# Kernel tuning notes

Hardware: AMD Instinct MI355X
Metric: run time of the kernel (lower is better)

The kernel has to match this reference:

```python
import jax, jax.numpy as jnp
from jax import lax
import numpy as np

jax.config.update("jax_enable_x64", True)  # coder state needs 32-bit unsigned range in int64

FULL = 1 << 32
HALF = FULL >> 1
QUARTER = HALF >> 1
THREE_Q = 3 * QUARTER
RANGE_MASK = FULL - 1
CTX_BITS = 8
N_STATES = 1 << CTX_BITS
STATE_MASK = N_STATES - 1
PRECISION = 12
TOTAL = 1 << PRECISION
MAXBITS = 1 << 21


def _context_freqs(bits):
    # Adaptive per-context P(bit=0) frequencies, sequential over the bit stream.
    def step(carry, bit):
        c0, c1, state = carry
        a = c0[state]
        b = c1[state]
        p0 = a.astype(jnp.float64) / (a + b).astype(jnp.float64)
        f = jnp.clip(jnp.rint(p0 * (TOTAL - 2)) + 1.0, 1.0, TOTAL - 1.0).astype(jnp.int64)
        c0 = c0.at[state].add(1 - bit)
        c1 = c1.at[state].add(bit)
        state = ((state << 1) | bit) & STATE_MASK
        return (c0, c1, state), f

    init = (jnp.ones(N_STATES, jnp.int64), jnp.ones(N_STATES, jnp.int64), jnp.int64(0))
    _, freqs = lax.scan(step, init, bits)
    return freqs


def _arith_encode(bits, freqs):
    # Binary arithmetic coder with carry-pending renormalization.
    def renorm_cond(c):
        low, high, pending, buf, ptr = c
        return (high < HALF) | (low >= HALF) | ((low >= QUARTER) & (high < THREE_Q))

    def renorm_body(c):
        low, high, pending, buf, ptr = c
        is_a = high < HALF                      # emit 0
        is_b = (~is_a) & (low >= HALF)          # emit 1
        do_emit = is_a | is_b
        outbit = is_b.astype(jnp.uint8)
        n_write = jnp.where(do_emit, 1 + pending, jnp.int64(0))

        def wbody(i, b):
            return b.at[ptr + i].set(jnp.where(i == 0, outbit, 1 - outbit))

        buf = lax.fori_loop(0, n_write, wbody, buf)
        ptr = ptr + n_write
        pending = jnp.where(do_emit, jnp.int64(0), pending + 1)
        shift = jnp.where(is_a, jnp.int64(0), jnp.where(is_b, jnp.int64(HALF), jnp.int64(QUARTER)))
        low = ((low - shift) << 1) & RANGE_MASK
        high = (((high - shift) << 1) & RANGE_MASK) | 1
        return (low, high, pending, buf, ptr)

    def step(carry, inp):
        low, high, pending, buf, ptr = carry
        bit, p0 = inp
        rng = high - low + 1
        split = low + (rng * p0) // TOTAL
        high = jnp.where(bit == 0, split - 1, high)
        low = jnp.where(bit == 0, low, split)
        carry = lax.while_loop(renorm_cond, renorm_body, (low, high, pending, buf, ptr))
        return carry, None

    init = (jnp.int64(0), jnp.int64(FULL - 1), jnp.int64(0),
            jnp.zeros(MAXBITS, jnp.uint8), jnp.int64(0))
    (low, high, pending, buf, ptr), _ = lax.scan(step, init, (bits, freqs))

    # flush: pending += 1 then emit final bit + pending complements
    pending = pending + 1
    final_bit = (low >= QUARTER).astype(jnp.uint8)
    buf = buf.at[ptr].set(final_bit)
    buf = lax.fori_loop(0, pending, lambda i, b: b.at[ptr + 1 + i].set(1 - final_bit), buf)
    ptr = ptr + 1 + pending

    # packbits MSB-first (bitorder='big'); trailing buffer bits are zero, matching numpy's zero-padding
    w = jnp.array([128, 64, 32, 16, 8, 4, 2, 1], jnp.int64)
    packed = (buf.reshape(-1, 8).astype(jnp.int64) * w).sum(-1).astype(jnp.uint8)
    return packed, ptr


def setup_inputs() -> dict:
    key = jax.random.key(0)
    raw = jax.random.randint(key, (1024, 1024), 0, 2)
    symbols = (2 * raw - 1).astype(jnp.float32)  # values in {-1, +1}
    return {"symbols": symbols}


def reference(symbols):
    bits = ((symbols.reshape(-1) + 1.0) * 0.5).astype(jnp.uint8).astype(jnp.int64)
    freqs = _context_freqs(bits)
    packed, nbits = _arith_encode(bits, freqs)
    return packed, nbits
```

## Files before the change

kernel.cpp:

```cpp
#include <hip/hip_runtime.h>
#include <hip/hip_bf16.h>


#define N_TOT (1 << 20)
#define BLK_ELEMS 4096
#define N_BLKS (N_TOT / BLK_ELEMS)
#define NLIMB 65552

__global__ void k_keys(const float* __restrict__ sym, unsigned short* __restrict__ keys) {
    int t = blockIdx.x * blockDim.x + threadIdx.x;
    if (t >= N_TOT) return;
    unsigned s = 0;
#pragma unroll
    for (int i = 1; i <= 8; ++i) {
        unsigned b = (t >= i) ? (sym[t - i] > 0.0f ? 1u : 0u) : 0u;
        s |= b << (i - 1);
    }
    unsigned bit = sym[t] > 0.0f ? 1u : 0u;
    keys[t] = (unsigned short)((s << 1) | bit);
}

__global__ void k_hist(const unsigned short* __restrict__ keys, unsigned* __restrict__ histG) {
    __shared__ unsigned h[512];
    for (int i = threadIdx.x; i < 512; i += blockDim.x) h[i] = 0;
    __syncthreads();
    int base = blockIdx.x * BLK_ELEMS;
    for (int i = threadIdx.x; i < BLK_ELEMS; i += blockDim.x)
        atomicAdd(&h[keys[base + i]], 1u);
    __syncthreads();
    for (int i = threadIdx.x; i < 512; i += blockDim.x)
        histG[blockIdx.x * 512 + i] = h[i];
}

__global__ void k_scan(const unsigned* __restrict__ histG, unsigned* __restrict__ offsG) {
    int k = blockIdx.x * blockDim.x + threadIdx.x;
    if (k >= 512) return;
    unsigned run = 0;
    for (int b = 0; b < N_BLKS; ++b) {
        offsG[b * 512 + k] = run;
        run += histG[b * 512 + k];
    }
}

__global__ __launch_bounds__(64) void k_freq(const unsigned short* __restrict__ keys,
                                             const unsigned* __restrict__ offsG,
                                             unsigned short* __restrict__ fb) {
    __shared__ unsigned cnt[512];
    int lane = threadIdx.x;
    for (int i = lane; i < 512; i += 64) cnt[i] = offsG[blockIdx.x * 512 + i];
    __syncthreads();
    int base = blockIdx.x * BLK_ELEMS;
    unsigned long long ltm = (1ull << lane) - 1ull;
    for (int c = 0; c < BLK_ELEMS / 64; ++c) {
        int t = base + c * 64 + lane;
        unsigned key = keys[t];
        unsigned bit = key & 1u;
        unsigned state = key >> 1;
        unsigned long long eq = ~0ull;
#pragma unroll
        for (int b = 0; b < 8; ++b) {
            unsigned long long mb = __ballot((state >> b) & 1u);
            eq &= ((state >> b) & 1u) ? mb : ~mb;
        }
        unsigned long long bb = __ballot(bit);
        unsigned long long same = eq & (bit ? bb : ~bb);
        unsigned long long sib  = eq & (bit ? ~bb : bb);
        unsigned base_same = cnt[key];
        unsigned base_sib  = cnt[key ^ 1u];
        __syncthreads();
        unsigned c_same = base_same + (unsigned)__popcll(same & ltm);
        unsigned c_sib  = base_sib  + (unsigned)__popcll(sib & ltm);
        unsigned long long a0 = 1ull + (unsigned long long)(bit ? c_sib : c_same);
        unsigned long long a1 = 1ull + (unsigned long long)(bit ? c_same : c_sib);
        double p0 = (double)a0 / (double)(a0 + a1);
        double fd = rint(p0 * 4094.0) + 1.0;
        fd = fd < 1.0 ? 1.0 : (fd > 4095.0 ? 4095.0 : fd);
        unsigned f = (unsigned)fd;
        fb[t] = (unsigned short)(f | (bit << 15));
        int hi = 63 - __builtin_clzll(same);
        if (lane == hi) cnt[key] = base_same + (unsigned)__popcll(same);
        __syncthreads();
    }
}

__global__ void k_zerol(unsigned long long* __restrict__ limb) {
    int i = blockIdx.x * 256 + threadIdx.x;
    if (i < NLIMB) limb[i] = 0ull;
}

#define SYM(W, FI, BP) \
  "s_bfe_u32 s22, " W ", " FI "\n\t"           \
  "s_mul_i32 s20, s24, s22\n\t"                \
  "s_mul_hi_u32 s21, s24, s22\n\t"             \
  "s_add_u32 s20, s20, s22\n\t"                \
  "s_addc_u32 s21, s21, 0\n\t"                                      \
  "s_lshr_b64 s[20:21], s[20:21], 12\n\t"      \
  "s_add_u32 s26, %[lo], s20\n\t"              \
  "s_add_u32 s27, s26, -1\n\t"                 \
  "s_bitcmp1_b32 " W ", " BP "\n\t"            \
  "s_cselect_b32 %[lo], s26, %[lo]\n\t"        \
  "s_cselect_b32 %[hi], %[hi], s27\n\t"        \
  "s_xor_b32 s28, %[lo], %[hi]\n\t"            \
  "s_flbit_i32_b32 s29, s28\n\t"               \
  "s_andn2_b32 s30, %[lo], %[hi]\n\t"          \
  "s_add_u32 s31, s29, 1\n\t"                                       \
  "s_lshl_b32 s30, s30, s31\n\t"               \
  "s_and_b32 s34, s30, 0x80000000\n\t"         \
  "s_not_b32 s32, s30\n\t"                                          \
  "s_flbit_i32_b32 s33, s32\n\t"               \
  "s_add_u32 s29, s29, s33\n\t"                \
  "s_add_u32 %[pp], %[pp], s29\n\t"                                 \
  "s_lshl_b32 %[lo], %[lo], s29\n\t"                                \
  "s_lshl_b32 %[hi], %[hi], s29\n\t"                                \
  "s_lshl_b32 s35, 1, s29\n\t"                                      \
  "s_xor_b32 %[lo], %[lo], s34\n\t"                                 \
  "s_add_u32 s35, s35, -1\n\t"                 \
  "s_add_u32 %[hi], %[hi], s35\n\t"                                 \
  "s_xor_b32 %[hi], %[hi], s34\n\t"                                 \
  "s_sub_u32 s24, %[hi], %[lo]\n\t"

#define SYM2(W) SYM(W, "0x000C0000", "15") SYM(W, "0x000C0010", "31")

__global__ __launch_bounds__(64) void k_enc4(const unsigned short* __restrict__ fb,
                                             uint4* __restrict__ bnd,
                                             unsigned* __restrict__ hdr) {
    if (threadIdx.x != 0 || blockIdx.x != 0) return;
    unsigned low = 0u, high = 0xFFFFFFFFu, pp = 0u;
    const uint4* pq = (const uint4*)fb;
    uint4 A = pq[0], B = pq[1];
    const int NC = N_TOT / 16;
    for (int cc = 0; cc < NC; ++cc) {
        if ((cc & 15) == 0) bnd[cc >> 4] = make_uint4(low, high, pp, 0u);
        unsigned w0 = __builtin_amdgcn_readfirstlane(A.x);
        unsigned w1 = __builtin_amdgcn_readfirstlane(A.y);
        unsigned w2 = __builtin_amdgcn_readfirstlane(A.z);
        unsigned w3 = __builtin_amdgcn_readfirstlane(A.w);
        unsigned w4 = __builtin_amdgcn_readfirstlane(B.x);
        unsigned w5 = __builtin_amdgcn_readfirstlane(B.y);
        unsigned w6 = __builtin_amdgcn_readfirstlane(B.z);
        unsigned w7 = __builtin_amdgcn_readfirstlane(B.w);
        if (cc + 1 < NC) { A = pq[2 * cc + 2]; B = pq[2 * cc + 3]; }
        asm volatile(
            "s_sub_u32 s24, %[hi], %[lo]\n\t"
            SYM2("%[w0]") SYM2("%[w1]") SYM2("%[w2]") SYM2("%[w3]")
            SYM2("%[w4]") SYM2("%[w5]") SYM2("%[w6]") SYM2("%[w7]")
            : [lo]"+s"(low), [hi]"+s"(high), [pp]"+s"(pp)
            : [w0]"s"(w0), [w1]"s"(w1), [w2]"s"(w2), [w3]"s"(w3),
              [w4]"s"(w4), [w5]"s"(w5), [w6]"s"(w6), [w7]"s"(w7)
            : "s20","s21","s22","s23","s24","s25","s26","s27","s28","s29",
              "s30","s31","s32","s33","s34","s35","scc");
    }
    hdr[1] = pp;
}

__global__ __launch_bounds__(256) void k_chunk(const unsigned short* __restrict__ fb,
                                               const uint4* __restrict__ bnd,
                                               const unsigned* __restrict__ hdr,
                                               unsigned long long* __restrict__ limb) {
    int c = blockIdx.x * 256 + threadIdx.x;
    uint4 s = bnd[c];
    unsigned low = s.x, high = s.y, pp = s.z;
    unsigned pend = hdr[1];
    const unsigned* fw = (const unsigned*)fb;
    int base = c * 256;
    for (int i = 0; i < 256; i += 2) {
        unsigned w = fw[(base + i) >> 1];
#pragma unroll
        for (int h = 0; h < 2; ++h) {
            unsigned val = (w >> (h * 16)) & 0xFFFFu;
            unsigned f = val & 0xFFFu;
            unsigned bitv = val >> 15;
            unsigned r = high - low;
            unsigned long long prod = (unsigned long long)r * f + f;
            unsigned d = (unsigned)(prod >> 12);
            unsigned split = low + d;
            if (bitv) {
                unsigned sh = pend - pp;
                unsigned long long v = (unsigned long long)d << (sh & 31u);
                unsigned j = sh >> 5;
                atomicAdd(&limb[j], v & 0xFFFFFFFFull);
                unsigned long long vh = v >> 32;
                if (vh) atomicAdd(&limb[j + 1], vh);
            }
            high = bitv ? high : (split - 1u);
            low  = bitv ? split : low;
            unsigned D = low ^ high;
            unsigned k = (unsigned)__builtin_clz(D);
            unsigned kp1 = k + 1u;
            unsigned m = (unsigned)__builtin_clz((~(low << kp1)) | (high << kp1));
            unsigned K = k + m;
            pp += K;
            unsigned sub = m ? 0x80000000u : 0u;
            low  = (low << K) ^ sub;
            high = ((high << K) + ((1u << K) - 1u)) ^ sub;
        }
    }
}

__global__ __launch_bounds__(64) void k_carry2(const unsigned long long* __restrict__ limb,
                                               unsigned* __restrict__ res,
                                               unsigned* __restrict__ hdr) {
    if (threadIdx.x != 0 || blockIdx.x != 0) return;
    unsigned long long c = 0ull;
    const uint4* lp = (const uint4*)limb;
    unsigned first = 0;
    for (int b = 0; b < NLIMB / 16; ++b) {
        uint4 q[8];
#pragma unroll
        for (int u = 0; u < 8; ++u) q[u] = lp[b * 8 + u];
#pragma unroll
        for (int u = 0; u < 8; ++u) {
            unsigned long long l0 = (unsigned long long)q[u].x | ((unsigned long long)q[u].y << 32);
            unsigned long long l1 = (unsigned long long)q[u].z | ((unsigned long long)q[u].w << 32);
            unsigned long long t = l0 + c;
            res[b * 16 + 2 * u] = (unsigned)t; c = t >> 32;
            t = l1 + c;
            res[b * 16 + 2 * u + 1] = (unsigned)t; c = t >> 32;
            if (b == 0 && u == 0) first = res[0];
        }
    }
    unsigned fbit = (first >> 30) & 1u;
    res[0] = 1u << (30u + fbit);
    hdr[0] = hdr[1] + 2u;
}

__global__ void k_out2(const unsigned* __restrict__ res,
                       const unsigned* __restrict__ hdr, int* __restrict__ out) {
    int q = blockIdx.x * blockDim.x + threadIdx.x;
    if (q > 262144) return;
    unsigned nbits = hdr[0];
    if (q == 262144) { out[q] = (int)nbits; return; }
    if ((unsigned)(8 * q) >= nbits) { out[q] = 0; return; }
    unsigned pend = nbits - 2u;
    unsigned t = pend + 24u - 8u * (unsigned)q;
    unsigned j = t >> 5, o = t & 31u;
    unsigned long long w = (unsigned long long)res[j] | ((unsigned long long)res[j + 1] << 32);
    out[q] = (int)((w >> o) & 0xFFu);
}

extern "C" void kernel_launch(void* const* d_in, const int* in_sizes, int n_in,
                              void* d_out, int out_size, void* d_ws, size_t ws_size,
                              hipStream_t stream) {
    (void)in_sizes; (void)n_in; (void)out_size; (void)ws_size;
    const float* sym = (const float*)d_in[0];
    int* out = (int*)d_out;
    char* ws = (char*)d_ws;
    unsigned*            hdr   = (unsigned*)(ws);
    unsigned*            histG = (unsigned*)(ws + 266240);
    unsigned*            offsG = (unsigned*)(ws + 790528);
    unsigned short*      keys  = (unsigned short*)(ws + 1314816);
    unsigned short*      fb    = (unsigned short*)(ws + 3411968);
    unsigned long long*  limb  = (unsigned long long*)(ws + 266240);
    unsigned*            res   = (unsigned*)(ws + 790656);
    uint4*               bnd   = (uint4*)(ws + 1314816);

    k_keys<<<N_TOT / 256, 256, 0, stream>>>(sym, keys);
    k_hist<<<N_BLKS, 256, 0, stream>>>(keys, histG);
    k_scan<<<1, 512, 0, stream>>>(histG, offsG);
    k_freq<<<N_BLKS, 64, 0, stream>>>(keys, offsG, fb);
    k_zerol<<<(NLIMB + 255) / 256, 256, 0, stream>>>(limb);
    k_enc4<<<1, 64, 0, stream>>>(fb, bnd, hdr);
    k_chunk<<<16, 256, 0, stream>>>(fb, bnd, hdr, limb);
    k_carry2<<<1, 64, 0, stream>>>(limb, res, hdr);
    k_out2<<<1025, 256, 0, stream>>>(res, hdr, out);
}
```

Before: 61.17 ms.

## Drop bit-count tracking from serial scalar encoder; recover it with parallel chunk pass and scan

The single-thread scalar arithmetic-coder pass no longer accumulates the output bit position. It only records low/high at chunk boundaries, and it now processes 32 symbols per iteration. A new parallel pass re-encodes each chunk to count its emitted bits, and a scan turns those counts into per-chunk bit offsets and the total for the final pass. The renormalization sequence is also shortened by folding the mask into a shift of high+1, and constants are moved into SGPRs. The aim is to shorten the serial critical path, which dominates runtime, at the cost of an extra parallel pass and two extra launches.

```diff
diff --git a/kernel.cpp b/kernel.cpp
--- a/kernel.cpp
+++ b/kernel.cpp
@@ -93,44 +93,42 @@
   "s_mul_i32 s20, s24, s22\n\t"                \
   "s_mul_hi_u32 s21, s24, s22\n\t"             \
   "s_add_u32 s20, s20, s22\n\t"                \
-  "s_addc_u32 s21, s21, 0\n\t"                                      \
+  "s_addc_u32 s21, s21, 0\n\t"                                             \
   "s_lshr_b64 s[20:21], s[20:21], 12\n\t"      \
   "s_add_u32 s26, %[lo], s20\n\t"              \
   "s_add_u32 s27, s26, -1\n\t"                 \
   "s_bitcmp1_b32 " W ", " BP "\n\t"            \
-  "s_cselect_b32 %[lo], s26, %[lo]\n\t"        \
-  "s_cselect_b32 %[hi], %[hi], s27\n\t"        \
-  "s_xor_b32 s28, %[lo], %[hi]\n\t"            \
+  "s_cselect_b32 %[lo], s26, %[lo]\n\t"                                    \
+  "s_cselect_b32 %[hi], %[hi], s27\n\t"                                    \
+  "s_xor_b32 s28, %[lo], %[hi]\n\t"                                        \
   "s_flbit_i32_b32 s29, s28\n\t"               \
-  "s_andn2_b32 s30, %[lo], %[hi]\n\t"          \
-  "s_add_u32 s31, s29, 1\n\t"                                       \
+  "s_andn2_b32 s30, %[lo], %[hi]\n\t"                                      \
+  "s_add_u32 s31, s29, 1\n\t"                                              \
   "s_lshl_b32 s30, s30, s31\n\t"               \
-  "s_and_b32 s34, s30, 0x80000000\n\t"         \
-  "s_not_b32 s32, s30\n\t"                                          \
+  "s_and_b32 s34, s30, %[msk]\n\t"             \
+  "s_not_b32 s32, s30\n\t"                                                 \
   "s_flbit_i32_b32 s33, s32\n\t"               \
   "s_add_u32 s29, s29, s33\n\t"                \
-  "s_add_u32 %[pp], %[pp], s29\n\t"                                 \
-  "s_lshl_b32 %[lo], %[lo], s29\n\t"                                \
-  "s_lshl_b32 %[hi], %[hi], s29\n\t"                                \
-  "s_lshl_b32 s35, 1, s29\n\t"                                      \
-  "s_xor_b32 %[lo], %[lo], s34\n\t"                                 \
-  "s_add_u32 s35, s35, -1\n\t"                 \
-  "s_add_u32 %[hi], %[hi], s35\n\t"                                 \
-  "s_xor_b32 %[hi], %[hi], s34\n\t"                                 \
+  "s_lshl_b32 %[lo], %[lo], s29\n\t"                                       \
+  "s_add_u32 %[hi], %[hi], 1\n\t"              \
+  "s_lshl_b32 %[hi], %[hi], s29\n\t"                                       \
+  "s_xor_b32 %[lo], %[lo], s34\n\t"                                        \
+  "s_add_u32 %[hi], %[hi], -1\n\t"             \
+  "s_xor_b32 %[hi], %[hi], s34\n\t"                                        \
   "s_sub_u32 s24, %[hi], %[lo]\n\t"
 
-#define SYM2(W) SYM(W, "0x000C0000", "15") SYM(W, "0x000C0010", "31")
-
-__global__ __launch_bounds__(64) void k_enc4(const unsigned short* __restrict__ fb,
-                                             uint4* __restrict__ bnd,
-                                             unsigned* __restrict__ hdr) {
+#define SYM2(W) SYM(W, "%[c0]", "15") SYM(W, "%[c1]", "31")
+
+__global__ __launch_bounds__(64) void k_enc5(const unsigned short* __restrict__ fb,
+                                             uint2* __restrict__ bnd) {
     if (threadIdx.x != 0 || blockIdx.x != 0) return;
-    unsigned low = 0u, high = 0xFFFFFFFFu, pp = 0u;
+    unsigned low = 0u, high = 0xFFFFFFFFu;
+    unsigned c0 = 0x000C0000u, c1 = 0x000C0010u, mk = 0x80000000u;
     const uint4* pq = (const uint4*)fb;
-    uint4 A = pq[0], B = pq[1];
-    const int NC = N_TOT / 16;
+    uint4 A = pq[0], B = pq[1], C = pq[2], D = pq[3];
+    const int NC = N_TOT / 32;
     for (int cc = 0; cc < NC; ++cc) {
-        if ((cc & 15) == 0) bnd[cc >> 4] = make_uint4(low, high, pp, 0u);
+        if ((cc & 7) == 0) bnd[cc >> 3] = make_uint2(low, high);
         unsigned w0 = __builtin_amdgcn_readfirstlane(A.x);
         unsigned w1 = __builtin_amdgcn_readfirstlane(A.y);
         unsigned w2 = __builtin_amdgcn_readfirstlane(A.z);
@@ -139,27 +137,107 @@
         unsigned w5 = __builtin_amdgcn_readfirstlane(B.y);
         unsigned w6 = __builtin_amdgcn_readfirstlane(B.z);
         unsigned w7 = __builtin_amdgcn_readfirstlane(B.w);
-        if (cc + 1 < NC) { A = pq[2 * cc + 2]; B = pq[2 * cc + 3]; }
+        unsigned w8 = __builtin_amdgcn_readfirstlane(C.x);
+        unsigned w9 = __builtin_amdgcn_readfirstlane(C.y);
+        unsigned wa = __builtin_amdgcn_readfirstlane(C.z);
+        unsigned wb = __builtin_amdgcn_readfirstlane(C.w);
+        unsigned wc = __builtin_amdgcn_readfirstlane(D.x);
+        unsigned wd = __builtin_amdgcn_readfirstlane(D.y);
+        unsigned we = __builtin_amdgcn_readfirstlane(D.z);
+        unsigned wf = __builtin_amdgcn_readfirstlane(D.w);
+        if (cc + 1 < NC) {
+            A = pq[4 * cc + 4]; B = pq[4 * cc + 5];
+            C = pq[4 * cc + 6]; D = pq[4 * cc + 7];
+        }
         asm volatile(
             "s_sub_u32 s24, %[hi], %[lo]\n\t"
             SYM2("%[w0]") SYM2("%[w1]") SYM2("%[w2]") SYM2("%[w3]")
             SYM2("%[w4]") SYM2("%[w5]") SYM2("%[w6]") SYM2("%[w7]")
-            : [lo]"+s"(low), [hi]"+s"(high), [pp]"+s"(pp)
+            SYM2("%[w8]") SYM2("%[w9]") SYM2("%[wa]") SYM2("%[wb]")
+            SYM2("%[wc]") SYM2("%[wd]") SYM2("%[we]") SYM2("%[wf]")
+            : [lo]"+s"(low), [hi]"+s"(high)
             : [w0]"s"(w0), [w1]"s"(w1), [w2]"s"(w2), [w3]"s"(w3),
-              [w4]"s"(w4), [w5]"s"(w5), [w6]"s"(w6), [w7]"s"(w7)
+              [w4]"s"(w4), [w5]"s"(w5), [w6]"s"(w6), [w7]"s"(w7),
+              [w8]"s"(w8), [w9]"s"(w9), [wa]"s"(wa), [wb]"s"(wb),
+              [wc]"s"(wc), [wd]"s"(wd), [we]"s"(we), [wf]"s"(wf),
+              [c0]"s"(c0), [c1]"s"(c1), [msk]"s"(mk)
             : "s20","s21","s22","s23","s24","s25","s26","s27","s28","s29",
               "s30","s31","s32","s33","s34","s35","scc");
     }
-    hdr[1] = pp;
-}
-
-__global__ __launch_bounds__(256) void k_chunk(const unsigned short* __restrict__ fb,
-                                               const uint4* __restrict__ bnd,
-                                               const unsigned* __restrict__ hdr,
-                                               unsigned long long* __restrict__ limb) {
+}
+
+__global__ __launch_bounds__(256) void k_chunkA(const unsigned short* __restrict__ fb,
+                                                const uint2* __restrict__ bnd,
+                                                unsigned* __restrict__ dpp) {
     int c = blockIdx.x * 256 + threadIdx.x;
-    uint4 s = bnd[c];
-    unsigned low = s.x, high = s.y, pp = s.z;
+    uint2 s = bnd[c];
+    unsigned low = s.x, high = s.y, pp = 0;
+    const unsigned* fw = (const unsigned*)fb;
+    int base = c * 256;
+    for (int i = 0; i < 256; i += 2) {
+        unsigned w = fw[(base + i) >> 1];
+#pragma unroll
+        for (int h = 0; h < 2; ++h) {
+            unsigned val = (w >> (h * 16)) & 0xFFFFu;
+            unsigned f = val & 0xFFFu;
+            unsigned bitv = val >> 15;
+            unsigned r = high - low;
+            unsigned long long prod = (unsigned long long)r * f + f;
+            unsigned d = (unsigned)(prod >> 12);
+            unsigned split = low + d;
+            high = bitv ? high : (split - 1u);
+            low  = bitv ? split : low;
+            unsigned D = low ^ high;
+            unsigned k = (unsigned)__builtin_clz(D);
+            unsigned kp1 = k + 1u;
+            unsigned m = (unsigned)__builtin_clz((~(low << kp1)) | (high << kp1));
+            unsigned K = k + m;
+            pp += K;
+            unsigned sub = m ? 0x80000000u : 0u;
+            low  = (low << K) ^ sub;
+            high = ((high << K) + ((1u << K) - 1u)) ^ sub;
+        }
+    }
+    dpp[c] = pp;
+}
+
+__global__ __launch_bounds__(256) void k_scan2(const unsigned* __restrict__ dpp,
+                                               unsigned* __restrict__ ppb,
+                                               unsigned* __restrict__ hdr) {
+    __shared__ unsigned part[256];
+    int t = threadIdx.x;
+    uint4 v[4];
+    const uint4* dp = (const uint4*)(dpp + t * 16);
+    unsigned s = 0;
+#pragma unroll
+    for (int i = 0; i < 4; ++i) { v[i] = dp[i]; s += v[i].x + v[i].y + v[i].z + v[i].w; }
+    part[t] = s;
+    __syncthreads();
+    if (t == 0) {
+        unsigned run = 0;
+        for (int i = 0; i < 256; ++i) { unsigned x = part[i]; part[i] = run; run += x; }
+        hdr[1] = run;
+    }
+    __syncthreads();
+    unsigned run = part[t];
+    unsigned* pb = ppb + t * 16;
+#pragma unroll
+    for (int i = 0; i < 4; ++i) {
+        pb[4 * i + 0] = run; run += v[i].x;
+        pb[4 * i + 1] = run; run += v[i].y;
+        pb[4 * i + 2] = run; run += v[i].z;
+        pb[4 * i + 3] = run; run += v[i].w;
+    }
+}
+
+__global__ __launch_bounds__(256) void k_chunkB(const unsigned short* __restrict__ fb,
+                                                const uint2* __restrict__ bnd,
+                                                const unsigned* __restrict__ ppb,
+                                                const unsigned* __restrict__ hdr,
+                                                unsigned long long* __restrict__ limb) {
+    int c = blockIdx.x * 256 + threadIdx.x;
+    uint2 s = bnd[c];
+    unsigned low = s.x, high = s.y, pp = ppb[c];
     unsigned pend = hdr[1];
     const unsigned* fw = (const unsigned*)fb;
     int base = c * 256;
@@ -252,15 +330,19 @@
     unsigned short*      fb    = (unsigned short*)(ws + 3411968);
     unsigned long long*  limb  = (unsigned long long*)(ws + 266240);
     unsigned*            res   = (unsigned*)(ws + 790656);
-    uint4*               bnd   = (uint4*)(ws + 1314816);
+    uint2*               bnd   = (uint2*)(ws + 1314816);
+    unsigned*            dpp   = (unsigned*)(ws + 1347584);
+    unsigned*            ppb   = (unsigned*)(ws + 1363968);
 
     k_keys<<<N_TOT / 256, 256, 0, stream>>>(sym, keys);
     k_hist<<<N_BLKS, 256, 0, stream>>>(keys, histG);
     k_scan<<<1, 512, 0, stream>>>(histG, offsG);
     k_freq<<<N_BLKS, 64, 0, stream>>>(keys, offsG, fb);
     k_zerol<<<(NLIMB + 255) / 256, 256, 0, stream>>>(limb);
-    k_enc4<<<1, 64, 0, stream>>>(fb, bnd, hdr);
-    k_chunk<<<16, 256, 0, stream>>>(fb, bnd, hdr, limb);
+    k_enc5<<<1, 64, 0, stream>>>(fb, bnd);
+    k_chunkA<<<16, 256, 0, stream>>>(fb, bnd, dpp);
+    k_scan2<<<1, 256, 0, stream>>>(dpp, ppb, hdr);
+    k_chunkB<<<16, 256, 0, stream>>>(fb, bnd, ppb, hdr, limb);
     k_carry2<<<1, 64, 0, stream>>>(limb, res, hdr);
     k_out2<<<1025, 256, 0, stream>>>(res, hdr, out);
 }
```

New measurement: 56.81 ms. 7.1% less time.
